# Kernel tuning notes

Measured on AMD Instinct MI355X. Metric: run time of the kernel, lower is better.

## Reference

```python
import jax, jax.numpy as jnp
import numpy as np

B, L, D = 8, 2048, 64
EPS = 1e-8


def setup_inputs() -> dict:
    key = jax.random.key(0)
    ks = jax.random.split(key, 7)
    s = 1.0 / np.sqrt(D)  # ~ torch Linear default init scale
    return {
        "x": jax.random.normal(ks[0], (B, L, D), dtype=jnp.float32),
        "B_w": jax.random.normal(ks[1], (D, D), dtype=jnp.float32) * s,
        "B_b": jax.random.normal(ks[2], (D,), dtype=jnp.float32) * s,
        "C_w": jax.random.normal(ks[3], (D, D), dtype=jnp.float32) * s,
        "C_b": jax.random.normal(ks[4], (D,), dtype=jnp.float32) * s,
        "V_w": jax.random.normal(ks[5], (D, D), dtype=jnp.float32) * s,
        "V_b": jax.random.normal(ks[6], (D,), dtype=jnp.float32) * s,
    }


def reference(x, B_w, B_b, C_w, C_b, V_w, V_b):
    # torch nn.Linear: y = x @ W.T + b
    BZ = jnp.einsum('bld,ed->ble', x, B_w) + B_b   # (B,L,D)
    CZ = jnp.einsum('bld,ed->ble', x, C_w) + C_b   # (B,L,D)
    scores = jnp.einsum('bld,bmd->blm', BZ, CZ)     # (B,L,L)
    attn = jax.nn.relu(scores)
    # note: normalization over dim=-2 (column sums), as in the original
    attn = attn / (attn.sum(axis=-2, keepdims=True) + EPS)
    VZ = jnp.einsum('bld,ed->ble', x, V_w) + V_b   # (B,L,D)
    out = jnp.einsum('blm,bmd->bld', attn, VZ)      # (B,L,D)
    return x + out
```

## Files before the change

kernel.cpp:

```cpp
#include <hip/hip_runtime.h>

typedef unsigned short u16;
typedef unsigned int u32;
typedef __bf16 bf16x8 __attribute__((ext_vector_type(8)));
typedef float f32x16 __attribute__((ext_vector_type(16)));
typedef const void __attribute__((address_space(1))) gvoid;
typedef void __attribute__((address_space(3))) lvoid;

#define GLOAD16(gp, lp) __builtin_amdgcn_global_load_lds((gvoid*)(gp), (lvoid*)(lp), 16, 0, 0)
#define POST_BARRIER_FENCE() do { __builtin_amdgcn_sched_barrier(0); asm volatile("" ::: "memory"); } while (0)

namespace {
constexpr int Ln = 2048;
constexpr float EPS = 1e-8f;
}

__device__ __forceinline__ u16 f2bf(float f) {
  __bf16 h = (__bf16)f;
  return __builtin_bit_cast(u16, h);
}

__device__ __forceinline__ u32 pk2(float lo, float hi) {
    u32 r;
    asm("v_cvt_pk_bf16_f32 %0, %1, %2" : "=v"(r) : "v"(lo), "v"(hi));
    return r;
}

__device__ __forceinline__ void half_swap(u32 a, u32 b, u32& na, u32& nb) {
    u32 sa = (u32)__shfl_xor((int)a, 32, 64);
    u32 sb = (u32)__shfl_xor((int)b, 32, 64);
    int hi = (threadIdx.x & 63) >> 5;
    na = hi ? a : sb;
    nb = hi ? sa : b;
}

__global__ __launch_bounds__(256) void proj_k(
    const float* __restrict__ x,
    const float* __restrict__ Bw, const float* __restrict__ Bb,
    const float* __restrict__ Cw, const float* __restrict__ Cb,
    const float* __restrict__ Vw, const float* __restrict__ Vb,
    u16* __restrict__ BZh, u16* __restrict__ CZh, u16* __restrict__ VZTh)
{
    const int tid = threadIdx.x;
    const int ln = tid & 31;
    const int g5 = (tid >> 5) & 1;
    const int w  = tid >> 6;
    const int row0 = blockIdx.x * 128 + w * 32;

    bf16x8 wf[3][2][4];
    const float* const Wp[3] = {Bw, Cw, Vw};
    #pragma unroll
    for (int m = 0; m < 3; ++m)
      #pragma unroll
      for (int e = 0; e < 2; ++e)
        #pragma unroll
        for (int c = 0; c < 4; ++c) {
            const float* p = Wp[m] + (e * 32 + ln) * 64 + c * 16 + g5 * 8;
            const float4 lo = *(const float4*)p;
            const float4 hi = *(const float4*)(p + 4);
            uint4 t4;
            t4.x = pk2(lo.x, lo.y); t4.y = pk2(lo.z, lo.w);
            t4.z = pk2(hi.x, hi.y); t4.w = pk2(hi.z, hi.w);
            wf[m][e][c] = __builtin_bit_cast(bf16x8, t4);
        }
    bf16x8 xf[4];
    {
        const float* xp = x + (row0 + ln) * 64 + g5 * 8;
        #pragma unroll
        for (int c = 0; c < 4; ++c) {
            const float4 lo = *(const float4*)(xp + c * 16);
            const float4 hi = *(const float4*)(xp + c * 16 + 4);
            uint4 t4;
            t4.x = pk2(lo.x, lo.y); t4.y = pk2(lo.z, lo.w);
            t4.z = pk2(hi.x, hi.y); t4.w = pk2(hi.z, hi.w);
            xf[c] = __builtin_bit_cast(bf16x8, t4);
        }
    }
    const int b   = row0 >> 11;
    const int l0b = row0 & 2047;
    const float* const biasBC[2] = {Bb, Cb};
    u16* const outBC[2] = {BZh, CZh};
    #pragma unroll
    for (int m = 0; m < 2; ++m) {
        #pragma unroll
        for (int e = 0; e < 2; ++e) {
            f32x16 st;
            #pragma unroll
            for (int q = 0; q < 4; ++q) {
                const float4 bv = *(const float4*)(biasBC[m] + e * 32 + q * 8 + g5 * 4);
                st[q*4+0] = bv.x; st[q*4+1] = bv.y; st[q*4+2] = bv.z; st[q*4+3] = bv.w;
            }
            #pragma unroll
            for (int c = 0; c < 4; ++c)
                st = __builtin_amdgcn_mfma_f32_32x32x16_bf16(wf[m][e][c], xf[c], st, 0, 0, 0);
            u16* op = outBC[m] + (row0 + ln) * 64 + e * 32 + g5 * 4;
            #pragma unroll
            for (int q = 0; q < 4; ++q) {
                uint2 pk;
                pk.x = pk2(st[q*4+0], st[q*4+1]);
                pk.y = pk2(st[q*4+2], st[q*4+3]);
                *(uint2*)(op + q * 8) = pk;
            }
        }
    }
    #pragma unroll
    for (int e = 0; e < 2; ++e) {
        const float vb = Vb[e * 32 + ln];
        f32x16 st;
        #pragma unroll
        for (int r = 0; r < 16; ++r) st[r] = vb;
        #pragma unroll
        for (int c = 0; c < 4; ++c)
            st = __builtin_amdgcn_mfma_f32_32x32x16_bf16(xf[c], wf[2][e][c], st, 0, 0, 0);
        u16* op = VZTh + (b * 64 + e * 32 + ln) * Ln + l0b + g5 * 4;
        #pragma unroll
        for (int q = 0; q < 4; ++q) {
            uint2 pk;
            pk.x = pk2(st[q*4+0], st[q*4+1]);
            pk.y = pk2(st[q*4+2], st[q*4+3]);
            *(uint2*)(op + q * 8) = pk;
        }
    }
}

__global__ __launch_bounds__(512) void denom_k(
    const u16* __restrict__ BZh, const u16* __restrict__ CZh,
    float* __restrict__ denp)
{
    __shared__ __attribute__((aligned(16))) char smem2[49152 + 1024];
    float* const red = (float*)(smem2 + 49152);
    const int tid = threadIdx.x;
    const int lane = tid & 63;
    const int ln = lane & 31;
    const int g5 = lane >> 5;
    const int w = tid >> 6;
    const int wm2 = w & 1, wl2 = w >> 1;
    const int flat = (int)blockIdx.z * 256 + (int)blockIdx.y * 32 + (int)blockIdx.x;
    const int nf = (flat & 7) * 64 + (flat >> 3);
    const int b = nf >> 6;
    const int rem = nf & 63;
    const int mb = (rem & 31) * 64;
    const int half = rem >> 5;
    const int l0h = half * 1024;
    const int wave_base = tid & ~63;

    bf16x8 af[4];
    {
        const u16* cp = CZh + ((b * Ln + mb + wm2 * 32 + ln) << 6) + g5 * 8;
        #pragma unroll
        for (int c = 0; c < 4; ++c) af[c] = *(const bf16x8*)(cp + c * 16);
    }
    auto stageD = [&](int t) {
        char* buf = smem2 + (t % 3) * 16384;
        #pragma unroll
        for (int it = 0; it < 2; ++it) {
            int j = (it << 9) + tid;
            int r = j >> 3;
            int u = (j & 7) ^ (r & 7);
            GLOAD16(BZh + ((b * Ln + l0h + t * 128 + r) << 6) + (u << 3),
                    buf + ((it << 9) + wave_base) * 16);
        }
    };
    stageD(0); stageD(1);
    __syncthreads();
    float accs[16];
    #pragma unroll
    for (int r = 0; r < 16; ++r) accs[r] = 0.f;
    const int lr = wl2 * 32 + ln;
    for (int t = 0; t < 8; ++t) {
        if (t > 0) {
            if (t < 7) asm volatile("s_waitcnt vmcnt(2)" ::: "memory");
            else       asm volatile("s_waitcnt vmcnt(0)" ::: "memory");
            __builtin_amdgcn_s_barrier();
            POST_BARRIER_FENCE();
        }
        if (t + 2 < 8) stageD(t + 2);
        const char* buf = smem2 + (t % 3) * 16384;
        f32x16 st = {};
        __builtin_amdgcn_s_setprio(1);
        #pragma unroll
        for (int c = 0; c < 4; ++c) {
            int un = (c << 1) | g5;
            bf16x8 bfr = *(const bf16x8*)(buf + (lr << 7) + ((un ^ (lr & 7)) << 4));
            st = __builtin_amdgcn_mfma_f32_32x32x16_bf16(af[c], bfr, st, 0, 0, 0);
        }
        __builtin_amdgcn_s_setprio(0);
        #pragma unroll
        for (int r = 0; r < 16; ++r) accs[r] += fmaxf(st[r], 0.f);
    }
    #pragma unroll
    for (int msk = 1; msk <= 16; msk <<= 1)
        #pragma unroll
        for (int r = 0; r < 16; ++r)
            accs[r] += __shfl_xor(accs[r], msk, 64);
    if (ln == 0) {
        #pragma unroll
        for (int r = 0; r < 16; ++r) {
            int mloc = wm2 * 32 + (r & 3) + ((r >> 2) << 3) + g5 * 4;
            red[mloc * 4 + wl2] = accs[r];
        }
    }
    __syncthreads();
    if (tid < 64)
        denp[(half * 8 + b) * Ln + mb + tid] =
            red[tid*4+0] + red[tid*4+1] + red[tid*4+2] + red[tid*4+3];
}

__global__ __launch_bounds__(512) void fused_out(
    const float* __restrict__ x,
    const u16* __restrict__ BZh, const u16* __restrict__ CZh,
    const u16* __restrict__ VZTh, const float* __restrict__ denp,
    float* __restrict__ out)
{
    __shared__ __attribute__((aligned(16))) char smem[114688];
    char* const BZs = smem;
    float* const denl = (float*)(smem + 8192);
    char* const bufs = smem + 16384;
    const int tid = threadIdx.x;
    const int lane = tid & 63;
    const int ln = lane & 31;
    const int g5 = lane >> 5;
    const int w = tid >> 6;
    const int wm = w & 3;
    const int wl = w >> 2;
    const int flat = (int)blockIdx.y * 32 + (int)blockIdx.x;
    const int nf = (flat & 7) * 32 + (flat >> 3);
    const int b = nf >> 5;
    const int l0 = (nf & 31) * 64;
    const int wave_base = tid & ~63;

    auto stage = [&](int t) {
        char* bufc = bufs + (t % 3) * 32768;
        char* vzb = bufc + 16384;
        const int m0s = t << 7;
        #pragma unroll
        for (int it = 0; it < 2; ++it) {
            int j = (it << 9) + tid;
            int r = j >> 3;
            int u = (j & 7) ^ (r & 7);
            GLOAD16(CZh + ((b * Ln + m0s + r) << 6) + (u << 3),
                    bufc + ((it << 9) + wave_base) * 16);
        }
        #pragma unroll
        for (int it = 0; it < 2; ++it) {
            int j = (it << 9) + tid;
            int r = j >> 4;
            int u = (j & 15) ^ (r & 7);
            GLOAD16(VZTh + ((b << 6) + r) * Ln + m0s + (u << 3),
                    vzb + ((it << 9) + wave_base) * 16);
        }
    };

    {
        int r = tid >> 3;
        int u = (tid & 7) ^ (r & 7);
        GLOAD16(BZh + ((b * Ln + l0 + r) << 6) + (u << 3), BZs + wave_base * 16);
    }
    {
        const float4 c0 = *(const float4*)(denp + b * Ln + tid * 4);
        const float4 c1 = *(const float4*)(denp + (8 + b) * Ln + tid * 4);
        float4 dv;
        dv.x = 1.f / (c0.x + c1.x + EPS);
        dv.y = 1.f / (c0.y + c1.y + EPS);
        dv.z = 1.f / (c0.z + c1.z + EPS);
        dv.w = 1.f / (c0.w + c1.w + EPS);
        *(float4*)(denl + tid * 4) = dv;
    }
    stage(0); stage(1);
    __syncthreads();

    bf16x8 bzf[4];
    {
        const int lr = wl * 32 + ln;
        #pragma unroll
        for (int c = 0; c < 4; ++c) {
            int un = (c << 1) | g5;
            bzf[c] = *(const bf16x8*)(BZs + (lr << 7) + ((un ^ (lr & 7)) << 4));
        }
    }
    f32x16 acc0 = {}, acc1 = {};
    const int mA = wm * 32 + ln;

    for (int t = 0; t < 16; ++t) {
        if (t > 0) {
            if (t < 15) asm volatile("s_waitcnt vmcnt(4)" ::: "memory");
            else        asm volatile("s_waitcnt vmcnt(0)" ::: "memory");
            __builtin_amdgcn_s_barrier();
            POST_BARRIER_FENCE();
        }
        if (t + 2 < 16) stage(t + 2);
        const char* cz = bufs + (t % 3) * 32768;
        const char* vz = cz + 16384;
        f32x16 st = {};
        __builtin_amdgcn_s_setprio(1);
        #pragma unroll
        for (int c = 0; c < 4; ++c) {
            int un = (c << 1) | g5;
            bf16x8 a = *(const bf16x8*)(cz + (mA << 7) + ((un ^ (mA & 7)) << 4));
            st = __builtin_amdgcn_mfma_f32_32x32x16_bf16(a, bzf[c], st, 0, 0, 0);
        }
        __builtin_amdgcn_s_setprio(0);
        const int mq0 = (t << 7) + wm * 32;
        u32 wv[8];
        #pragma unroll
        for (int q = 0; q < 4; ++q) {
            const float4 dq = *(const float4*)(denl + mq0 + q * 8 + g5 * 4);
            float p0 = fmaxf(st[q*4+0], 0.f) * dq.x;
            float p1 = fmaxf(st[q*4+1], 0.f) * dq.y;
            float p2 = fmaxf(st[q*4+2], 0.f) * dq.z;
            float p3 = fmaxf(st[q*4+3], 0.f) * dq.w;
            wv[q*2+0] = pk2(p0, p1);
            wv[q*2+1] = pk2(p2, p3);
        }
        u32 f0w0, f0w1, f0w2, f0w3, f1w0, f1w1, f1w2, f1w3;
        half_swap(wv[2], wv[0], f0w2, f0w0);
        half_swap(wv[3], wv[1], f0w3, f0w1);
        half_swap(wv[6], wv[4], f1w2, f1w0);
        half_swap(wv[7], wv[5], f1w3, f1w1);
        bf16x8 pf0, pf1;
        { uint4 t4; t4.x=f0w0; t4.y=f0w1; t4.z=f0w2; t4.w=f0w3; pf0 = __builtin_bit_cast(bf16x8, t4); }
        { uint4 t4; t4.x=f1w0; t4.y=f1w1; t4.z=f1w2; t4.w=f1w3; pf1 = __builtin_bit_cast(bf16x8, t4); }
        const int un00 = (wm << 2) | g5;
        const int un01 = (wm << 2) | 2 | g5;
        __builtin_amdgcn_s_setprio(1);
        {
            bf16x8 av;
            av = *(const bf16x8*)(vz + (ln << 8) + ((un00 ^ (ln & 7)) << 4));
            acc0 = __builtin_amdgcn_mfma_f32_32x32x16_bf16(av, pf0, acc0, 0, 0, 0);
            av = *(const bf16x8*)(vz + (ln << 8) + ((un01 ^ (ln & 7)) << 4));
            acc0 = __builtin_amdgcn_mfma_f32_32x32x16_bf16(av, pf1, acc0, 0, 0, 0);
            av = *(const bf16x8*)(vz + ((32 + ln) << 8) + ((un00 ^ (ln & 7)) << 4));
            acc1 = __builtin_amdgcn_mfma_f32_32x32x16_bf16(av, pf0, acc1, 0, 0, 0);
            av = *(const bf16x8*)(vz + ((32 + ln) << 8) + ((un01 ^ (ln & 7)) << 4));
            acc1 = __builtin_amdgcn_mfma_f32_32x32x16_bf16(av, pf1, acc1, 0, 0, 0);
        }
        __builtin_amdgcn_s_setprio(0);
    }

    __syncthreads();
    float* red = (float*)(bufs);
    constexpr int LSTR = 36;
    constexpr int SSTR = 64 * LSTR;
    if (wm >= 2) {
        float* base = red + (wl * 2 + (wm - 2)) * SSTR + lane * LSTR;
        #pragma unroll
        for (int r = 0; r < 16; ++r) { base[r] = acc0[r]; base[16 + r] = acc1[r]; }
    }
    __syncthreads();
    if (wm < 2) {
        float* base = red + (wl * 2 + wm) * SSTR + lane * LSTR;
        #pragma unroll
        for (int r = 0; r < 16; ++r) { acc0[r] += base[r]; acc1[r] += base[16 + r]; }
    }
    __syncthreads();
    if (wm == 1) {
        float* base = red + (4 + wl) * SSTR + lane * LSTR;
        #pragma unroll
        for (int r = 0; r < 16; ++r) { base[r] = acc0[r]; base[16 + r] = acc1[r]; }
    }
    __syncthreads();
    float* lout = (float*)(smem);
    if (wm == 0) {
        float* base = red + (4 + wl) * SSTR + lane * LSTR;
        #pragma unroll
        for (int r = 0; r < 16; ++r) { acc0[r] += base[r]; acc1[r] += base[16 + r]; }
        const int lrow = wl * 32 + ln;
        #pragma unroll
        for (int q = 0; q < 4; ++q) {
            const int d0 = q * 8 + g5 * 4;
            float4 v0;
            v0.x = acc0[q*4+0]; v0.y = acc0[q*4+1]; v0.z = acc0[q*4+2]; v0.w = acc0[q*4+3];
            *(float4*)(lout + lrow * 68 + d0) = v0;
            float4 v1;
            v1.x = acc1[q*4+0]; v1.y = acc1[q*4+1]; v1.z = acc1[q*4+2]; v1.w = acc1[q*4+3];
            *(float4*)(lout + lrow * 68 + 32 + d0) = v1;
        }
    }
    __syncthreads();
    {
        const int row = tid >> 3;
        const int dc = (tid & 7) * 8;
        const int g = (b * Ln + l0 + row) * 64 + dc;
        float4 o0 = *(const float4*)(lout + row * 68 + dc);
        float4 o1 = *(const float4*)(lout + row * 68 + dc + 4);
        const float4 x0 = *(const float4*)(x + g);
        const float4 x1 = *(const float4*)(x + g + 4);
        o0.x += x0.x; o0.y += x0.y; o0.z += x0.z; o0.w += x0.w;
        o1.x += x1.x; o1.y += x1.y; o1.z += x1.z; o1.w += x1.w;
        *(float4*)(out + g) = o0;
        *(float4*)(out + g + 4) = o1;
    }
}

extern "C" void kernel_launch(void* const* d_in, const int* in_sizes, int n_in,
                              void* d_out, int out_size, void* d_ws, size_t ws_size,
                              hipStream_t stream) {
    const float* x  = (const float*)d_in[0];
    const float* Bw = (const float*)d_in[1];
    const float* Bb = (const float*)d_in[2];
    const float* Cw = (const float*)d_in[3];
    const float* Cb = (const float*)d_in[4];
    const float* Vw = (const float*)d_in[5];
    const float* Vb = (const float*)d_in[6];
    float* out = (float*)d_out;
    char* wsb = (char*)d_ws;
    u16* BZh  = (u16*)wsb;
    u16* CZh  = (u16*)(wsb + (2u << 20));
    u16* VZTh = (u16*)(wsb + (4u << 20));
    float* denp = (float*)(wsb + (6u << 20));

    proj_k<<<dim3(128), 256, 0, stream>>>(x, Bw, Bb, Cw, Cb, Vw, Vb, BZh, CZh, VZTh);
    denom_k<<<dim3(32, 8, 2), 512, 0, stream>>>(BZh, CZh, denp);
    fused_out<<<dim3(32, 8), 512, 0, stream>>>(x, BZh, CZh, VZTh, denp, out);
}
```

Baseline: 51.70 us.

## Replace LDS-staged pipelines with direct register double-buffered global loads

Both denom_k and fused_out drop the global_load_lds triple-buffered shared-memory staging and barriers. Each wave now loads its bf16 MFMA operand fragments straight from global memory into registers, with double buffering. denom_k no longer splits L into two halves: it launches 256 blocks, each covering the full 2048 rows, and writes a single column-sum array. The goal is to remove barrier and LDS traffic and to shrink shared memory to raise occupancy. The cost is more VGPRs, redundant global loads across waves (served from cache), and less parallelism in denom_k.

```diff
diff --git a/kernel.cpp b/kernel.cpp
--- a/kernel.cpp
+++ b/kernel.cpp
@@ -4,20 +4,10 @@
 typedef unsigned int u32;
 typedef __bf16 bf16x8 __attribute__((ext_vector_type(8)));
 typedef float f32x16 __attribute__((ext_vector_type(16)));
-typedef const void __attribute__((address_space(1))) gvoid;
-typedef void __attribute__((address_space(3))) lvoid;
-
-#define GLOAD16(gp, lp) __builtin_amdgcn_global_load_lds((gvoid*)(gp), (lvoid*)(lp), 16, 0, 0)
-#define POST_BARRIER_FENCE() do { __builtin_amdgcn_sched_barrier(0); asm volatile("" ::: "memory"); } while (0)
 
 namespace {
 constexpr int Ln = 2048;
 constexpr float EPS = 1e-8f;
-}
-
-__device__ __forceinline__ u16 f2bf(float f) {
-  __bf16 h = (__bf16)f;
-  return __builtin_bit_cast(u16, h);
 }
 
 __device__ __forceinline__ u32 pk2(float lo, float hi) {
@@ -125,24 +115,19 @@
 
 __global__ __launch_bounds__(512) void denom_k(
     const u16* __restrict__ BZh, const u16* __restrict__ CZh,
-    float* __restrict__ denp)
+    float* __restrict__ colsum)
 {
-    __shared__ __attribute__((aligned(16))) char smem2[49152 + 1024];
-    float* const red = (float*)(smem2 + 49152);
+    __shared__ float red[64][5];
     const int tid = threadIdx.x;
     const int lane = tid & 63;
     const int ln = lane & 31;
     const int g5 = lane >> 5;
     const int w = tid >> 6;
-    const int wm2 = w & 1, wl2 = w >> 1;
-    const int flat = (int)blockIdx.z * 256 + (int)blockIdx.y * 32 + (int)blockIdx.x;
-    const int nf = (flat & 7) * 64 + (flat >> 3);
-    const int b = nf >> 6;
-    const int rem = nf & 63;
-    const int mb = (rem & 31) * 64;
-    const int half = rem >> 5;
-    const int l0h = half * 1024;
-    const int wave_base = tid & ~63;
+    const int wm2 = w & 1, wl4 = w >> 1;
+    const int bx = (int)blockIdx.x;
+    const int nf = (bx & 7) * 32 + (bx >> 3);
+    const int b = nf >> 5;
+    const int mb = (nf & 31) * 64;
 
     bf16x8 af[4];
     {
@@ -150,40 +135,26 @@
         #pragma unroll
         for (int c = 0; c < 4; ++c) af[c] = *(const bf16x8*)(cp + c * 16);
     }
-    auto stageD = [&](int t) {
-        char* buf = smem2 + (t % 3) * 16384;
-        #pragma unroll
-        for (int it = 0; it < 2; ++it) {
-            int j = (it << 9) + tid;
-            int r = j >> 3;
-            int u = (j & 7) ^ (r & 7);
-            GLOAD16(BZh + ((b * Ln + l0h + t * 128 + r) << 6) + (u << 3),
-                    buf + ((it << 9) + wave_base) * 16);
-        }
+    const u16* const bp0 = BZh + ((b * Ln + wl4 * 32 + ln) << 6) + g5 * 8;
+    auto loadB = [&](int it, bf16x8* dst) {
+        const u16* bp = bp0 + ((it * 128) << 6);
+        #pragma unroll
+        for (int c = 0; c < 4; ++c) dst[c] = *(const bf16x8*)(bp + c * 16);
     };
-    stageD(0); stageD(1);
-    __syncthreads();
+    bf16x8 bF[2][4];
+    loadB(0, bF[0]);
     float accs[16];
     #pragma unroll
     for (int r = 0; r < 16; ++r) accs[r] = 0.f;
-    const int lr = wl2 * 32 + ln;
-    for (int t = 0; t < 8; ++t) {
-        if (t > 0) {
-            if (t < 7) asm volatile("s_waitcnt vmcnt(2)" ::: "memory");
-            else       asm volatile("s_waitcnt vmcnt(0)" ::: "memory");
-            __builtin_amdgcn_s_barrier();
-            POST_BARRIER_FENCE();
-        }
-        if (t + 2 < 8) stageD(t + 2);
-        const char* buf = smem2 + (t % 3) * 16384;
+    #pragma unroll
+    for (int it = 0; it < 16; ++it) {
+        const int cur = it & 1;
+        if (it < 15) loadB(it + 1, bF[cur ^ 1]);
         f32x16 st = {};
         __builtin_amdgcn_s_setprio(1);
         #pragma unroll
-        for (int c = 0; c < 4; ++c) {
-            int un = (c << 1) | g5;
-            bf16x8 bfr = *(const bf16x8*)(buf + (lr << 7) + ((un ^ (lr & 7)) << 4));
-            st = __builtin_amdgcn_mfma_f32_32x32x16_bf16(af[c], bfr, st, 0, 0, 0);
-        }
+        for (int c = 0; c < 4; ++c)
+            st = __builtin_amdgcn_mfma_f32_32x32x16_bf16(af[c], bF[cur][c], st, 0, 0, 0);
         __builtin_amdgcn_s_setprio(0);
         #pragma unroll
         for (int r = 0; r < 16; ++r) accs[r] += fmaxf(st[r], 0.f);
@@ -196,26 +167,24 @@
     if (ln == 0) {
         #pragma unroll
         for (int r = 0; r < 16; ++r) {
-            int mloc = wm2 * 32 + (r & 3) + ((r >> 2) << 3) + g5 * 4;
-            red[mloc * 4 + wl2] = accs[r];
+            const int moff = (r & 3) + ((r >> 2) << 3) + g5 * 4;
+            red[wm2 * 32 + moff][wl4] = accs[r];
         }
     }
     __syncthreads();
     if (tid < 64)
-        denp[(half * 8 + b) * Ln + mb + tid] =
-            red[tid*4+0] + red[tid*4+1] + red[tid*4+2] + red[tid*4+3];
+        colsum[b * Ln + mb + tid] =
+            red[tid][0] + red[tid][1] + red[tid][2] + red[tid][3];
 }
 
 __global__ __launch_bounds__(512) void fused_out(
     const float* __restrict__ x,
     const u16* __restrict__ BZh, const u16* __restrict__ CZh,
-    const u16* __restrict__ VZTh, const float* __restrict__ denp,
+    const u16* __restrict__ VZTh, const float* __restrict__ colsum,
     float* __restrict__ out)
 {
-    __shared__ __attribute__((aligned(16))) char smem[114688];
-    char* const BZs = smem;
-    float* const denl = (float*)(smem + 8192);
-    char* const bufs = smem + 16384;
+    __shared__ __attribute__((aligned(16))) char smem[63488];
+    float* const denl = (float*)smem;
     const int tid = threadIdx.x;
     const int lane = tid & 63;
     const int ln = lane & 31;
@@ -223,84 +192,59 @@
     const int w = tid >> 6;
     const int wm = w & 3;
     const int wl = w >> 2;
-    const int flat = (int)blockIdx.y * 32 + (int)blockIdx.x;
-    const int nf = (flat & 7) * 32 + (flat >> 3);
+    const int bx = (int)blockIdx.x;
+    const int nf = (bx & 7) * 32 + (bx >> 3);
     const int b = nf >> 5;
     const int l0 = (nf & 31) * 64;
-    const int wave_base = tid & ~63;
-
-    auto stage = [&](int t) {
-        char* bufc = bufs + (t % 3) * 32768;
-        char* vzb = bufc + 16384;
-        const int m0s = t << 7;
-        #pragma unroll
-        for (int it = 0; it < 2; ++it) {
-            int j = (it << 9) + tid;
-            int r = j >> 3;
-            int u = (j & 7) ^ (r & 7);
-            GLOAD16(CZh + ((b * Ln + m0s + r) << 6) + (u << 3),
-                    bufc + ((it << 9) + wave_base) * 16);
-        }
-        #pragma unroll
-        for (int it = 0; it < 2; ++it) {
-            int j = (it << 9) + tid;
-            int r = j >> 4;
-            int u = (j & 15) ^ (r & 7);
-            GLOAD16(VZTh + ((b << 6) + r) * Ln + m0s + (u << 3),
-                    vzb + ((it << 9) + wave_base) * 16);
-        }
+
+    {
+        const float4 cs = *(const float4*)(colsum + b * Ln + tid * 4);
+        float4 dv;
+        dv.x = 1.f / (cs.x + EPS); dv.y = 1.f / (cs.y + EPS);
+        dv.z = 1.f / (cs.z + EPS); dv.w = 1.f / (cs.w + EPS);
+        *(float4*)(denl + tid * 4) = dv;
+    }
+    bf16x8 bzf[4];
+    {
+        const u16* bp = BZh + ((b * Ln + l0 + wl * 32 + ln) << 6) + g5 * 8;
+        #pragma unroll
+        for (int c = 0; c < 4; ++c) bzf[c] = *(const bf16x8*)(bp + c * 16);
+    }
+    __syncthreads();
+
+    const u16* const cp0 = CZh + ((b * Ln + wm * 32 + ln) << 6) + g5 * 8;
+    const u16* const vp0 = VZTh + ((b << 6) + ln) * Ln + wm * 32 + g5 * 8;
+    const u16* const vp1 = vp0 + (Ln << 5);
+
+    auto loadA = [&](int t, bf16x8* dst) {
+        const u16* p = cp0 + ((t * 128) << 6);
+        #pragma unroll
+        for (int c = 0; c < 4; ++c) dst[c] = *(const bf16x8*)(p + c * 16);
     };
-
-    {
-        int r = tid >> 3;
-        int u = (tid & 7) ^ (r & 7);
-        GLOAD16(BZh + ((b * Ln + l0 + r) << 6) + (u << 3), BZs + wave_base * 16);
-    }
-    {
-        const float4 c0 = *(const float4*)(denp + b * Ln + tid * 4);
-        const float4 c1 = *(const float4*)(denp + (8 + b) * Ln + tid * 4);
-        float4 dv;
-        dv.x = 1.f / (c0.x + c1.x + EPS);
-        dv.y = 1.f / (c0.y + c1.y + EPS);
-        dv.z = 1.f / (c0.z + c1.z + EPS);
-        dv.w = 1.f / (c0.w + c1.w + EPS);
-        *(float4*)(denl + tid * 4) = dv;
-    }
-    stage(0); stage(1);
-    __syncthreads();
-
-    bf16x8 bzf[4];
-    {
-        const int lr = wl * 32 + ln;
-        #pragma unroll
-        for (int c = 0; c < 4; ++c) {
-            int un = (c << 1) | g5;
-            bzf[c] = *(const bf16x8*)(BZs + (lr << 7) + ((un ^ (lr & 7)) << 4));
-        }
-    }
+    auto loadV = [&](int t, bf16x8* dst) {
+        const u16* p0 = vp0 + t * 128;
+        const u16* p1 = vp1 + t * 128;
+        dst[0] = *(const bf16x8*)p0;
+        dst[1] = *(const bf16x8*)(p0 + 16);
+        dst[2] = *(const bf16x8*)p1;
+        dst[3] = *(const bf16x8*)(p1 + 16);
+    };
+
+    bf16x8 aF[2][4], vF[2][4];
+    loadA(0, aF[0]); loadV(0, vF[0]);
     f32x16 acc0 = {}, acc1 = {};
-    const int mA = wm * 32 + ln;
-
+
+    #pragma unroll
     for (int t = 0; t < 16; ++t) {
-        if (t > 0) {
-            if (t < 15) asm volatile("s_waitcnt vmcnt(4)" ::: "memory");
-            else        asm volatile("s_waitcnt vmcnt(0)" ::: "memory");
-            __builtin_amdgcn_s_barrier();
-            POST_BARRIER_FENCE();
-        }
-        if (t + 2 < 16) stage(t + 2);
-        const char* cz = bufs + (t % 3) * 32768;
-        const char* vz = cz + 16384;
+        const int cur = t & 1;
+        if (t < 15) { loadA(t + 1, aF[cur ^ 1]); loadV(t + 1, vF[cur ^ 1]); }
         f32x16 st = {};
         __builtin_amdgcn_s_setprio(1);
         #pragma unroll
-        for (int c = 0; c < 4; ++c) {
-            int un = (c << 1) | g5;
-            bf16x8 a = *(const bf16x8*)(cz + (mA << 7) + ((un ^ (mA & 7)) << 4));
-            st = __builtin_amdgcn_mfma_f32_32x32x16_bf16(a, bzf[c], st, 0, 0, 0);
-        }
+        for (int c = 0; c < 4; ++c)
+            st = __builtin_amdgcn_mfma_f32_32x32x16_bf16(aF[cur][c], bzf[c], st, 0, 0, 0);
         __builtin_amdgcn_s_setprio(0);
-        const int mq0 = (t << 7) + wm * 32;
+        const int mq0 = t * 128 + wm * 32;
         u32 wv[8];
         #pragma unroll
         for (int q = 0; q < 4; ++q) {
@@ -320,25 +264,16 @@
         bf16x8 pf0, pf1;
         { uint4 t4; t4.x=f0w0; t4.y=f0w1; t4.z=f0w2; t4.w=f0w3; pf0 = __builtin_bit_cast(bf16x8, t4); }
         { uint4 t4; t4.x=f1w0; t4.y=f1w1; t4.z=f1w2; t4.w=f1w3; pf1 = __builtin_bit_cast(bf16x8, t4); }
-        const int un00 = (wm << 2) | g5;
-        const int un01 = (wm << 2) | 2 | g5;
         __builtin_amdgcn_s_setprio(1);
-        {
-            bf16x8 av;
-            av = *(const bf16x8*)(vz + (ln << 8) + ((un00 ^ (ln & 7)) << 4));
-            acc0 = __builtin_amdgcn_mfma_f32_32x32x16_bf16(av, pf0, acc0, 0, 0, 0);
-            av = *(const bf16x8*)(vz + (ln << 8) + ((un01 ^ (ln & 7)) << 4));
-            acc0 = __builtin_amdgcn_mfma_f32_32x32x16_bf16(av, pf1, acc0, 0, 0, 0);
-            av = *(const bf16x8*)(vz + ((32 + ln) << 8) + ((un00 ^ (ln & 7)) << 4));
-            acc1 = __builtin_amdgcn_mfma_f32_32x32x16_bf16(av, pf0, acc1, 0, 0, 0);
-            av = *(const bf16x8*)(vz + ((32 + ln) << 8) + ((un01 ^ (ln & 7)) << 4));
-            acc1 = __builtin_amdgcn_mfma_f32_32x32x16_bf16(av, pf1, acc1, 0, 0, 0);
-        }
+        acc0 = __builtin_amdgcn_mfma_f32_32x32x16_bf16(vF[cur][0], pf0, acc0, 0, 0, 0);
+        acc0 = __builtin_amdgcn_mfma_f32_32x32x16_bf16(vF[cur][1], pf1, acc0, 0, 0, 0);
+        acc1 = __builtin_amdgcn_mfma_f32_32x32x16_bf16(vF[cur][2], pf0, acc1, 0, 0, 0);
+        acc1 = __builtin_amdgcn_mfma_f32_32x32x16_bf16(vF[cur][3], pf1, acc1, 0, 0, 0);
         __builtin_amdgcn_s_setprio(0);
     }
 
     __syncthreads();
-    float* red = (float*)(bufs);
+    float* red = (float*)(smem + 8192);
     constexpr int LSTR = 36;
     constexpr int SSTR = 64 * LSTR;
     if (wm >= 2) {
@@ -359,7 +294,7 @@
         for (int r = 0; r < 16; ++r) { base[r] = acc0[r]; base[16 + r] = acc1[r]; }
     }
     __syncthreads();
-    float* lout = (float*)(smem);
+    float* lout = (float*)smem;
     if (wm == 0) {
         float* base = red + (4 + wl) * SSTR + lane * LSTR;
         #pragma unroll
@@ -407,9 +342,9 @@
     u16* BZh  = (u16*)wsb;
     u16* CZh  = (u16*)(wsb + (2u << 20));
     u16* VZTh = (u16*)(wsb + (4u << 20));
-    float* denp = (float*)(wsb + (6u << 20));
+    float* colsum = (float*)(wsb + (6u << 20));
 
     proj_k<<<dim3(128), 256, 0, stream>>>(x, Bw, Bb, Cw, Cb, Vw, Vb, BZh, CZh, VZTh);
-    denom_k<<<dim3(32, 8, 2), 512, 0, stream>>>(BZh, CZh, denp);
-    fused_out<<<dim3(32, 8), 512, 0, stream>>>(x, BZh, CZh, VZTh, denp, out);
-}
+    denom_k<<<dim3(256), 512, 0, stream>>>(BZh, CZh, colsum);
+    fused_out<<<dim3(256), 512, 0, stream>>>(x, BZh, CZh, VZTh, colsum, out);
+}
```

Measured after the change: 67.60 us. +30.7%, slower.

## Load CZ/BZ fragments directly to registers and simplify fused_out reduction/epilogue

Applied to the files above, without the earlier changes.

In fused_out, the CZ and BZ tiles now go straight from global memory into double-buffered register fragments instead of being staged through LDS. Only VZT still uses the LDS triple buffer, which halves shared memory use. The cross-wave reduction collapses into one store/sum round, and the residual add writes straight from the accumulators, dropping an LDS transpose and several barriers. proj_k is also regridded to smaller blocks, and the explicit vmcnt waits are removed, so correct ordering of the LDS DMA now relies on the compiler.

```diff
diff --git a/kernel.cpp b/kernel.cpp
--- a/kernel.cpp
+++ b/kernel.cpp
@@ -15,11 +15,6 @@
 constexpr float EPS = 1e-8f;
 }
 
-__device__ __forceinline__ u16 f2bf(float f) {
-  __bf16 h = (__bf16)f;
-  return __builtin_bit_cast(u16, h);
-}
-
 __device__ __forceinline__ u32 pk2(float lo, float hi) {
     u32 r;
     asm("v_cvt_pk_bf16_f32 %0, %1, %2" : "=v"(r) : "v"(lo), "v"(hi));
@@ -34,7 +29,7 @@
     nb = hi ? sa : b;
 }
 
-__global__ __launch_bounds__(256) void proj_k(
+__global__ __launch_bounds__(128) void proj_k(
     const float* __restrict__ x,
     const float* __restrict__ Bw, const float* __restrict__ Bb,
     const float* __restrict__ Cw, const float* __restrict__ Cb,
@@ -45,7 +40,7 @@
     const int ln = tid & 31;
     const int g5 = (tid >> 5) & 1;
     const int w  = tid >> 6;
-    const int row0 = blockIdx.x * 128 + w * 32;
+    const int row0 = blockIdx.x * 64 + w * 32;
 
     bf16x8 wf[3][2][4];
     const float* const Wp[3] = {Bw, Cw, Vw};
@@ -212,10 +207,9 @@
     const u16* __restrict__ VZTh, const float* __restrict__ denp,
     float* __restrict__ out)
 {
-    __shared__ __attribute__((aligned(16))) char smem[114688];
-    char* const BZs = smem;
-    float* const denl = (float*)(smem + 8192);
-    char* const bufs = smem + 16384;
+    __shared__ __attribute__((aligned(16))) char smem[57344];
+    float* const denl = (float*)smem;
+    char* const bufs = smem + 8192;
     const int tid = threadIdx.x;
     const int lane = tid & 63;
     const int ln = lane & 31;
@@ -223,39 +217,30 @@
     const int w = tid >> 6;
     const int wm = w & 3;
     const int wl = w >> 2;
-    const int flat = (int)blockIdx.y * 32 + (int)blockIdx.x;
-    const int nf = (flat & 7) * 32 + (flat >> 3);
+    const int bx = (int)blockIdx.x;
+    const int nf = (bx & 7) * 32 + (bx >> 3);
     const int b = nf >> 5;
     const int l0 = (nf & 31) * 64;
     const int wave_base = tid & ~63;
 
     auto stage = [&](int t) {
-        char* bufc = bufs + (t % 3) * 32768;
-        char* vzb = bufc + 16384;
-        const int m0s = t << 7;
-        #pragma unroll
-        for (int it = 0; it < 2; ++it) {
-            int j = (it << 9) + tid;
-            int r = j >> 3;
-            int u = (j & 7) ^ (r & 7);
-            GLOAD16(CZh + ((b * Ln + m0s + r) << 6) + (u << 3),
-                    bufc + ((it << 9) + wave_base) * 16);
-        }
+        char* vzb = bufs + (t % 3) * 16384;
         #pragma unroll
         for (int it = 0; it < 2; ++it) {
             int j = (it << 9) + tid;
             int r = j >> 4;
-            int u = (j & 15) ^ (r & 7);
-            GLOAD16(VZTh + ((b << 6) + r) * Ln + m0s + (u << 3),
+            int uu = (j & 15) ^ (r & 7);
+            GLOAD16(VZTh + ((b << 6) + r) * Ln + (t << 7) + (uu << 3),
                     vzb + ((it << 9) + wave_base) * 16);
         }
     };
-
-    {
-        int r = tid >> 3;
-        int u = (tid & 7) ^ (r & 7);
-        GLOAD16(BZh + ((b * Ln + l0 + r) << 6) + (u << 3), BZs + wave_base * 16);
-    }
+    const u16* const cp0 = CZh + ((b * Ln + wm * 32 + ln) << 6) + g5 * 8;
+    auto loadA = [&](int t, bf16x8* dst) {
+        const u16* p = cp0 + ((t * 128) << 6);
+        #pragma unroll
+        for (int c = 0; c < 4; ++c) dst[c] = *(const bf16x8*)(p + c * 16);
+    };
+
     {
         const float4 c0 = *(const float4*)(denp + b * Ln + tid * 4);
         const float4 c1 = *(const float4*)(denp + (8 + b) * Ln + tid * 4);
@@ -266,39 +251,32 @@
         dv.w = 1.f / (c0.w + c1.w + EPS);
         *(float4*)(denl + tid * 4) = dv;
     }
-    stage(0); stage(1);
-    __syncthreads();
-
     bf16x8 bzf[4];
     {
-        const int lr = wl * 32 + ln;
-        #pragma unroll
-        for (int c = 0; c < 4; ++c) {
-            int un = (c << 1) | g5;
-            bzf[c] = *(const bf16x8*)(BZs + (lr << 7) + ((un ^ (lr & 7)) << 4));
-        }
-    }
+        const u16* bp = BZh + ((b * Ln + l0 + wl * 32 + ln) << 6) + g5 * 8;
+        #pragma unroll
+        for (int c = 0; c < 4; ++c) bzf[c] = *(const bf16x8*)(bp + c * 16);
+    }
+    stage(0); stage(1);
+    bf16x8 aF[2][4];
+    loadA(0, aF[0]);
+    __syncthreads();
+
     f32x16 acc0 = {}, acc1 = {};
-    const int mA = wm * 32 + ln;
-
+    #pragma unroll
     for (int t = 0; t < 16; ++t) {
+        const int cur = t & 1;
         if (t > 0) {
-            if (t < 15) asm volatile("s_waitcnt vmcnt(4)" ::: "memory");
-            else        asm volatile("s_waitcnt vmcnt(0)" ::: "memory");
             __builtin_amdgcn_s_barrier();
             POST_BARRIER_FENCE();
         }
         if (t + 2 < 16) stage(t + 2);
-        const char* cz = bufs + (t % 3) * 32768;
-        const char* vz = cz + 16384;
+        if (t + 1 < 16) loadA(t + 1, aF[cur ^ 1]);
         f32x16 st = {};
         __builtin_amdgcn_s_setprio(1);
         #pragma unroll
-        for (int c = 0; c < 4; ++c) {
-            int un = (c << 1) | g5;
-            bf16x8 a = *(const bf16x8*)(cz + (mA << 7) + ((un ^ (mA & 7)) << 4));
-            st = __builtin_amdgcn_mfma_f32_32x32x16_bf16(a, bzf[c], st, 0, 0, 0);
-        }
+        for (int c = 0; c < 4; ++c)
+            st = __builtin_amdgcn_mfma_f32_32x32x16_bf16(aF[cur][c], bzf[c], st, 0, 0, 0);
         __builtin_amdgcn_s_setprio(0);
         const int mq0 = (t << 7) + wm * 32;
         u32 wv[8];
@@ -320,6 +298,7 @@
         bf16x8 pf0, pf1;
         { uint4 t4; t4.x=f0w0; t4.y=f0w1; t4.z=f0w2; t4.w=f0w3; pf0 = __builtin_bit_cast(bf16x8, t4); }
         { uint4 t4; t4.x=f1w0; t4.y=f1w1; t4.z=f1w2; t4.w=f1w3; pf1 = __builtin_bit_cast(bf16x8, t4); }
+        const char* vz = bufs + (t % 3) * 16384;
         const int un00 = (wm << 2) | g5;
         const int un01 = (wm << 2) | 2 | g5;
         __builtin_amdgcn_s_setprio(1);
@@ -338,57 +317,37 @@
     }
 
     __syncthreads();
-    float* red = (float*)(bufs);
+    float* red = (float*)smem;
     constexpr int LSTR = 36;
     constexpr int SSTR = 64 * LSTR;
-    if (wm >= 2) {
-        float* base = red + (wl * 2 + (wm - 2)) * SSTR + lane * LSTR;
+    if (wm != 0) {
+        float* base = red + ((wm - 1) * 2 + wl) * SSTR + lane * LSTR;
         #pragma unroll
         for (int r = 0; r < 16; ++r) { base[r] = acc0[r]; base[16 + r] = acc1[r]; }
     }
     __syncthreads();
-    if (wm < 2) {
-        float* base = red + (wl * 2 + wm) * SSTR + lane * LSTR;
-        #pragma unroll
-        for (int r = 0; r < 16; ++r) { acc0[r] += base[r]; acc1[r] += base[16 + r]; }
-    }
-    __syncthreads();
-    if (wm == 1) {
-        float* base = red + (4 + wl) * SSTR + lane * LSTR;
-        #pragma unroll
-        for (int r = 0; r < 16; ++r) { base[r] = acc0[r]; base[16 + r] = acc1[r]; }
-    }
-    __syncthreads();
-    float* lout = (float*)(smem);
     if (wm == 0) {
-        float* base = red + (4 + wl) * SSTR + lane * LSTR;
-        #pragma unroll
-        for (int r = 0; r < 16; ++r) { acc0[r] += base[r]; acc1[r] += base[16 + r]; }
-        const int lrow = wl * 32 + ln;
+        #pragma unroll
+        for (int s = 0; s < 3; ++s) {
+            float* base = red + (s * 2 + wl) * SSTR + lane * LSTR;
+            #pragma unroll
+            for (int r = 0; r < 16; ++r) { acc0[r] += base[r]; acc1[r] += base[16 + r]; }
+        }
+        const int row = b * Ln + l0 + wl * 32 + ln;
         #pragma unroll
         for (int q = 0; q < 4; ++q) {
             const int d0 = q * 8 + g5 * 4;
-            float4 v0;
-            v0.x = acc0[q*4+0]; v0.y = acc0[q*4+1]; v0.z = acc0[q*4+2]; v0.w = acc0[q*4+3];
-            *(float4*)(lout + lrow * 68 + d0) = v0;
-            float4 v1;
-            v1.x = acc1[q*4+0]; v1.y = acc1[q*4+1]; v1.z = acc1[q*4+2]; v1.w = acc1[q*4+3];
-            *(float4*)(lout + lrow * 68 + 32 + d0) = v1;
-        }
-    }
-    __syncthreads();
-    {
-        const int row = tid >> 3;
-        const int dc = (tid & 7) * 8;
-        const int g = (b * Ln + l0 + row) * 64 + dc;
-        float4 o0 = *(const float4*)(lout + row * 68 + dc);
-        float4 o1 = *(const float4*)(lout + row * 68 + dc + 4);
-        const float4 x0 = *(const float4*)(x + g);
-        const float4 x1 = *(const float4*)(x + g + 4);
-        o0.x += x0.x; o0.y += x0.y; o0.z += x0.z; o0.w += x0.w;
-        o1.x += x1.x; o1.y += x1.y; o1.z += x1.z; o1.w += x1.w;
-        *(float4*)(out + g) = o0;
-        *(float4*)(out + g + 4) = o1;
+            const float4 x0 = *(const float4*)(x + row * 64 + d0);
+            float4 o0;
+            o0.x = x0.x + acc0[q*4+0]; o0.y = x0.y + acc0[q*4+1];
+            o0.z = x0.z + acc0[q*4+2]; o0.w = x0.w + acc0[q*4+3];
+            *(float4*)(out + row * 64 + d0) = o0;
+            const float4 x1 = *(const float4*)(x + row * 64 + 32 + d0);
+            float4 o1;
+            o1.x = x1.x + acc1[q*4+0]; o1.y = x1.y + acc1[q*4+1];
+            o1.z = x1.z + acc1[q*4+2]; o1.w = x1.w + acc1[q*4+3];
+            *(float4*)(out + row * 64 + 32 + d0) = o1;
+        }
     }
 }
 
@@ -409,7 +368,7 @@
     u16* VZTh = (u16*)(wsb + (4u << 20));
     float* denp = (float*)(wsb + (6u << 20));
 
-    proj_k<<<dim3(128), 256, 0, stream>>>(x, Bw, Bb, Cw, Cb, Vw, Vb, BZh, CZh, VZTh);
+    proj_k<<<dim3(256), 128, 0, stream>>>(x, Bw, Bb, Cw, Cb, Vw, Vb, BZh, CZh, VZTh);
     denom_k<<<dim3(32, 8, 2), 512, 0, stream>>>(BZh, CZh, denp);
-    fused_out<<<dim3(32, 8), 512, 0, stream>>>(x, BZh, CZh, VZTh, denp, out);
-}
+    fused_out<<<dim3(256), 512, 0, stream>>>(x, BZh, CZh, VZTh, denp, out);
+}
```

Measured after the change: 56.57 us. 9.4% more time.
